# Performance work log

Hardware: AMD Instinct MI355X
Metric: run time of the kernel (lower is better)

The kernel has to match this reference:

```python
import jax, jax.numpy as jnp
import numpy as np

N_FFT = 200; HOP = 100; N_FREQ = N_FFT // 2 + 1  # 101
EMB = 256; HEADS = 8; DHEAD = EMB // HEADS; DEPTH = 4
N_CH = 23; B = 256; TS = 2000
MASK_RATIO = 0.9


def _layernorm(x, s, b):
    mu = jnp.mean(x, -1, keepdims=True)
    var = jnp.mean((x - mu) ** 2, -1, keepdims=True)
    return (x - mu) * jax.lax.rsqrt(var + 1e-5) * s + b


def _posenc(T, d):
    pos = jnp.arange(T, dtype=jnp.float32)[:, None]
    div = jnp.exp(jnp.arange(0, d, 2, dtype=jnp.float32) * (-np.log(10000.0) / d))
    pe = jnp.zeros((T, d), jnp.float32)
    pe = pe.at[:, 0::2].set(jnp.sin(pos * div))
    pe = pe.at[:, 1::2].set(jnp.cos(pos * div))
    return pe


def setup_inputs() -> dict:
    key = jax.random.key(0)
    ks = jax.random.split(key, 12)
    def n(k, shape):
        return (jax.random.normal(k, shape) * 0.02).astype(jnp.float32)
    T = 1 + (TS - N_FFT) // HOP  # 19
    S = N_CH * T                 # 437
    return dict(
        x=jax.random.normal(ks[0], (B, N_CH, TS), jnp.float32),
        mask_noise=jax.random.uniform(ks[1], (B, S, EMB), dtype=jnp.float32),
        W_proj=n(ks[2], (N_FREQ, EMB)), b_proj=jnp.zeros((EMB,), jnp.float32),
        channel_tokens=n(ks[3], (N_CH, EMB)),
        ln1_s=jnp.ones((DEPTH, EMB), jnp.float32), ln1_b=jnp.zeros((DEPTH, EMB), jnp.float32),
        Wq=n(ks[4], (DEPTH, EMB, EMB)), Wk=n(ks[5], (DEPTH, EMB, EMB)),
        Wv=n(ks[6], (DEPTH, EMB, EMB)), Wo=n(ks[7], (DEPTH, EMB, EMB)),
        bo=jnp.zeros((DEPTH, EMB), jnp.float32),
        ln2_s=jnp.ones((DEPTH, EMB), jnp.float32), ln2_b=jnp.zeros((DEPTH, EMB), jnp.float32),
        W1=n(ks[8], (DEPTH, EMB, 4 * EMB)), b1=jnp.zeros((DEPTH, 4 * EMB), jnp.float32),
        W2=n(ks[9], (DEPTH, 4 * EMB, EMB)), b2=jnp.zeros((DEPTH, EMB), jnp.float32),
    )


def _forward(x, mask_noise, W_proj, b_proj, channel_tokens,
             ln1_s, ln1_b, Wq, Wk, Wv, Wo, bo, ln2_s, ln2_b, W1, b1, W2, b2):
    Bb, C, ts = x.shape
    T = 1 + (ts - N_FFT) // HOP
    # ---- vectorized per-channel STFT (rect window, center=False, onesided) ----
    idx = jnp.arange(T)[:, None] * HOP + jnp.arange(N_FFT)[None, :]  # [T, n_fft]
    frames = x[:, :, idx]                                            # [B,C,T,n_fft]
    spec = jnp.abs(jnp.fft.rfft(frames, axis=-1)).astype(x.dtype)    # [B,C,T,F]
    # patch embedding (Linear over freq), channel token, positional encoding
    emb = spec @ W_proj + b_proj                                     # [B,C,T,E]
    emb = emb + channel_tokens[:C][None, :, None, :]
    emb = emb + _posenc(T, emb.shape[-1])[None, None]
    emb = emb.reshape(Bb, C * T, -1)                                 # [B,S,E]
    # ---- random masking (mask_ratio=0.9 as hard-coded in forward) ----
    mask = mask_noise < MASK_RATIO
    masked = jnp.where(mask, jnp.zeros((), emb.dtype), emb)
    # ---- LinearAttentionTransformer (non-causal linear attention, pre-norm) ----
    h = masked
    for l in range(DEPTH):
        y = _layernorm(h, ln1_s[l], ln1_b[l])
        S = y.shape[1]
        q = (y @ Wq[l]).reshape(Bb, S, HEADS, DHEAD).transpose(0, 2, 1, 3)
        k = (y @ Wk[l]).reshape(Bb, S, HEADS, DHEAD).transpose(0, 2, 1, 3)
        v = (y @ Wv[l]).reshape(Bb, S, HEADS, DHEAD).transpose(0, 2, 1, 3)
        q = jax.nn.softmax(q, axis=-1) * (DHEAD ** -0.5)
        k = jax.nn.softmax(k, axis=2)  # softmax over sequence
        ctx = jnp.einsum('bhnd,bhne->bhde', k, v)     # [B,H,d,d] global context
        att = jnp.einsum('bhnd,bhde->bhne', q, ctx)   # [B,H,S,d]
        att = att.transpose(0, 2, 1, 3).reshape(Bb, S, EMB)
        h = h + att @ Wo[l] + bo[l]
        y = _layernorm(h, ln2_s[l], ln2_b[l])
        h = h + jax.nn.gelu(y @ W1[l] + b1[l]) @ W2[l] + b2[l]
    return emb, masked, h, mask


def reference(x, mask_noise, W_proj, b_proj, channel_tokens,
              ln1_s, ln1_b, Wq, Wk, Wv, Wo, bo, ln2_s, ln2_b, W1, b1, W2, b2):
    return _forward(x, mask_noise, W_proj, b_proj, channel_tokens,
                    ln1_s, ln1_b, Wq, Wk, Wv, Wo, bo, ln2_s, ln2_b, W1, b1, W2, b2)
```

## Files before the change

kernel.cpp:

```cpp
#include <hip/hip_runtime.h>

#define BB    256
#define NCH   23
#define TT    19
#define SS    437
#define BSR   111872
#define EMBD  256
#define NHEAD 8
#define DH    32
#define NFREQ 101
#define NFFT  200
#define HOPSZ 100
#define TSLEN 2000
#define HID   1024
#define NDEPTH 4
#define NTOK  28639232
#define QKVW  768
#define WL    786432

typedef __attribute__((ext_vector_type(8))) __bf16 bf16x8;
typedef __attribute__((ext_vector_type(4))) float  f32x4;

__device__ __forceinline__ float gelu_f(float x){
    return 0.5f*x*(1.0f + tanhf(0.7978845608028654f*(x + 0.044715f*x*x*x)));
}
__device__ __forceinline__ unsigned short f2b(float f){
    unsigned u = __float_as_uint(f);
    return (unsigned short)((u + 0x7FFFu + ((u >> 16) & 1u)) >> 16);
}
__device__ __forceinline__ float b2f(unsigned short h){
    return __uint_as_float(((unsigned)h) << 16);
}

__device__ __forceinline__ void swz_tile(int& bx, int& by){
    int nx = gridDim.x, nwg = nx * gridDim.y;
    int lid = blockIdx.y * nx + blockIdx.x;
    int q = nwg >> 3, r = nwg & 7;
    int xcd = lid & 7, off = lid >> 3;
    int wgid = (xcd < r ? xcd*(q+1) : r*(q+1) + (xcd-r)*q) + off;
    bx = wgid % nx; by = wgid / nx;
}

__global__ void init_twb(unsigned short* __restrict__ tw){
    int i = blockIdx.x*256 + threadIdx.x;
    if(i >= 256*256) return;
    int n = i >> 8, k = i & 255;
    float v = 0.f;
    if(k < NFFT){
        if(n <= 100){
            int ph = (n * k) % NFFT;
            v = cosf(6.283185307179586f * (float)ph / (float)NFFT);
        } else if(n >= 128 && n <= 228){
            int ph = ((n - 128) * k) % NFFT;
            v = sinf(6.283185307179586f * (float)ph / (float)NFFT);
        }
    }
    tw[i] = f2b(v);
}

__global__ void init_pe(float* __restrict__ pe){
    int i = blockIdx.x*256 + threadIdx.x;
    if(i >= TT*EMBD) return;
    int t = i / EMBD, e = i % EMBD;
    int j = e >> 1;
    float div = expf((float)(2*j) * (-9.210340371976184f/256.0f));
    float ang = (float)t * div;
    pe[i] = (e & 1) ? cosf(ang) : sinf(ang);
}

__global__ void wprep_proj(const float* __restrict__ Wp, unsigned short* __restrict__ Wt){
    int i = blockIdx.x*256 + threadIdx.x;
    if(i >= 256*128) return;
    int e = i >> 7, k = i & 127;
    Wt[i] = f2b(k < NFREQ ? Wp[(size_t)k*EMBD + e] : 0.f);
}

__global__ void wprep_qkv(const float* __restrict__ Wq, const float* __restrict__ Wk,
                          const float* __restrict__ Wv, unsigned short* __restrict__ wbuf){
    long i = (long)blockIdx.x*256 + threadIdx.x;
    if(i >= (long)NDEPTH*QKVW*EMBD) return;
    int l = (int)(i / (QKVW*EMBD));
    int rem = (int)(i % (QKVW*EMBD));
    int n = rem >> 8, k = rem & 255;
    const float* W = (n < 256) ? Wq : (n < 512) ? Wk : Wv;
    wbuf[(size_t)l*WL + rem] = f2b(W[(size_t)l*65536 + (size_t)k*256 + (n & 255)]);
}
__global__ void wprep_wo(const float* __restrict__ Wo, unsigned short* __restrict__ wbuf){
    int i = blockIdx.x*256 + threadIdx.x;
    if(i >= NDEPTH*65536) return;
    int l = i >> 16, rem = i & 65535;
    int n = rem >> 8, k = rem & 255;
    wbuf[(size_t)l*WL + 196608 + rem] = f2b(Wo[(size_t)l*65536 + (size_t)k*256 + n]);
}
__global__ void wprep_w1(const float* __restrict__ W1, unsigned short* __restrict__ wbuf){
    long i = (long)blockIdx.x*256 + threadIdx.x;
    if(i >= (long)NDEPTH*262144) return;
    int l = (int)(i >> 18), rem = (int)(i & 262143);
    int n = rem >> 8, k = rem & 255;
    wbuf[(size_t)l*WL + 262144 + rem] = f2b(W1[(size_t)l*262144 + (size_t)k*1024 + n]);
}
__global__ void wprep_w2(const float* __restrict__ W2, unsigned short* __restrict__ wbuf){
    long i = (long)blockIdx.x*256 + threadIdx.x;
    if(i >= (long)NDEPTH*262144) return;
    int l = (int)(i >> 18), rem = (int)(i & 262143);
    int n = rem >> 10, k = rem & 1023;
    wbuf[(size_t)l*WL + 524288 + rem] = f2b(W2[(size_t)l*262144 + (size_t)k*256 + n]);
}

__global__ void frames_bf16(const float* __restrict__ x, unsigned short* __restrict__ fr){
    for(long i = (long)blockIdx.x*blockDim.x + threadIdx.x; i < (long)BSR*256;
        i += (long)gridDim.x*blockDim.x){
        int  k   = (int)(i & 255);
        long row = i >> 8;
        int  t   = (int)(row % TT);
        long bc  = row / TT;
        float v = (k < NFFT) ? x[bc*(long)TSLEN + (long)t*HOPSZ + k] : 0.f;
        fr[i] = f2b(v);
    }
}

__global__ void combine_bf16(const float* __restrict__ dft, unsigned short* __restrict__ sp){
    for(long i = (long)blockIdx.x*blockDim.x + threadIdx.x; i < (long)BSR*128;
        i += (long)gridDim.x*blockDim.x){
        int  f   = (int)(i & 127);
        long row = i >> 7;
        float v = 0.f;
        if(f < NFREQ){
            float c = dft[row*256 + f];
            float s = dft[row*256 + 128 + f];
            v = sqrtf(c*c + s*s);
        }
        sp[i] = f2b(v);
    }
}

template<int MODE>
__global__ __launch_bounds__(256) void gemm_mfma(
    const unsigned short* __restrict__ A, const unsigned short* __restrict__ Bt,
    const float* __restrict__ bias, void* __restrict__ Cv,
    const float* __restrict__ Cin, int M, int N, int K)
{
    __shared__ __align__(16) unsigned short As[128*64];
    __shared__ __align__(16) unsigned short Bs[128*64];
    const int tid = threadIdx.x;
    const int w = tid >> 6, l = tid & 63;
    int bx, by; swz_tile(bx, by);
    const int m0 = by * 128, n0 = bx * 128;
    const int wr = w >> 1, wc = w & 1;
    f32x4 acc[4][4];
    #pragma unroll
    for(int i=0;i<4;++i)
        #pragma unroll
        for(int jj=0;jj<4;++jj) acc[i][jj] = (f32x4){0.f,0.f,0.f,0.f};

    const int srow0 = w*32 + (l>>3);
    const int sgrp  = l & 7;

    for(int k0 = 0; k0 < K; k0 += 64){
        #pragma unroll
        for(int it=0; it<4; ++it){
            int row  = srow0 + it*8;
            int colA = ((sgrp ^ (row & 7)) << 3);
            const unsigned short* ga = A  + (size_t)(m0+row)*K + k0 + colA;
            const unsigned short* gb = Bt + (size_t)(n0+row)*K + k0 + colA;
            __builtin_amdgcn_global_load_lds(
                (__attribute__((address_space(1))) void*)ga,
                (__attribute__((address_space(3))) void*)(As + w*2048 + it*512),
                16, 0, 0);
            __builtin_amdgcn_global_load_lds(
                (__attribute__((address_space(1))) void*)gb,
                (__attribute__((address_space(3))) void*)(Bs + w*2048 + it*512),
                16, 0, 0);
        }
        __syncthreads();
        #pragma unroll
        for(int kk=0; kk<2; ++kk){
            bf16x8 af[4], bfr[4];
            #pragma unroll
            for(int mi=0;mi<4;++mi){
                int row = wr*64 + mi*16 + (l & 15);
                int grp = kk*4 + (l >> 4);
                af[mi] = *(const bf16x8*)&As[row*64 + ((grp ^ (row&7))<<3)];
            }
            #pragma unroll
            for(int ni=0;ni<4;++ni){
                int row = wc*64 + ni*16 + (l & 15);
                int grp = kk*4 + (l >> 4);
                bfr[ni] = *(const bf16x8*)&Bs[row*64 + ((grp ^ (row&7))<<3)];
            }
            #pragma unroll
            for(int mi=0;mi<4;++mi)
                #pragma unroll
                for(int ni=0;ni<4;++ni)
                    acc[mi][ni] = __builtin_amdgcn_mfma_f32_16x16x32_bf16(
                        af[mi], bfr[ni], acc[mi][ni], 0, 0, 0);
        }
        __syncthreads();
    }
    const int cn  = l & 15;
    const int cr4 = (l >> 4) * 4;
    if(MODE == 2 || MODE == 3){
        unsigned short* C = (unsigned short*)Cv;
        #pragma unroll
        for(int ni=0;ni<4;++ni){
            int n = n0 + wc*64 + ni*16 + cn;
            float bn = (MODE==2) ? bias[n] : 0.f;
            #pragma unroll
            for(int mi=0;mi<4;++mi){
                int mB = m0 + wr*64 + mi*16 + cr4;
                #pragma unroll
                for(int r=0;r<4;++r){
                    float v = acc[mi][ni][r];
                    C[(size_t)(mB+r)*N + n] = f2b(MODE==2 ? gelu_f(v + bn) : v);
                }
            }
        }
    } else {
        float* C = (float*)Cv;
        #pragma unroll
        for(int ni=0;ni<4;++ni){
            int n = n0 + wc*64 + ni*16 + cn;
            float bn = (MODE==1) ? bias[n] : 0.0f;
            #pragma unroll
            for(int mi=0;mi<4;++mi){
                int mB = m0 + wr*64 + mi*16 + cr4;
                #pragma unroll
                for(int r=0;r<4;++r){
                    size_t off = (size_t)(mB+r)*N + n;
                    if(MODE==0) C[off] = acc[mi][ni][r];
                    else        C[off] = Cin[off] + acc[mi][ni][r] + bn;
                }
            }
        }
    }
}

__global__ __launch_bounds__(256) void gemm_emb(
    const unsigned short* __restrict__ A, const unsigned short* __restrict__ Bt,
    const float* __restrict__ bp, const float* __restrict__ ctok,
    const float* __restrict__ pe, const float* __restrict__ noise,
    float* __restrict__ o_emb, float* __restrict__ o_masked,
    float* __restrict__ o_mask, float* __restrict__ bufH)
{
    const int K = 128, N = 256;
    __shared__ __align__(16) unsigned short As[128*64];
    __shared__ __align__(16) unsigned short Bs[128*64];
    const int tid = threadIdx.x;
    const int w = tid >> 6, l = tid & 63;
    int bx, by; swz_tile(bx, by);
    const int m0 = by * 128, n0 = bx * 128;
    const int wr = w >> 1, wc = w & 1;
    f32x4 acc[4][4];
    #pragma unroll
    for(int i=0;i<4;++i)
        #pragma unroll
        for(int jj=0;jj<4;++jj) acc[i][jj] = (f32x4){0.f,0.f,0.f,0.f};
    const int srow0 = w*32 + (l>>3);
    const int sgrp  = l & 7;
    for(int k0 = 0; k0 < K; k0 += 64){
        #pragma unroll
        for(int it=0; it<4; ++it){
            int row  = srow0 + it*8;
            int colA = ((sgrp ^ (row & 7)) << 3);
            const unsigned short* ga = A  + (size_t)(m0+row)*K + k0 + colA;
            const unsigned short* gb = Bt + (size_t)(n0+row)*K + k0 + colA;
            __builtin_amdgcn_global_load_lds(
                (__attribute__((address_space(1))) void*)ga,
                (__attribute__((address_space(3))) void*)(As + w*2048 + it*512),
                16, 0, 0);
            __builtin_amdgcn_global_load_lds(
                (__attribute__((address_space(1))) void*)gb,
                (__attribute__((address_space(3))) void*)(Bs + w*2048 + it*512),
                16, 0, 0);
        }
        __syncthreads();
        #pragma unroll
        for(int kk=0; kk<2; ++kk){
            bf16x8 af[4], bfr[4];
            #pragma unroll
            for(int mi=0;mi<4;++mi){
                int row = wr*64 + mi*16 + (l & 15);
                int grp = kk*4 + (l >> 4);
                af[mi] = *(const bf16x8*)&As[row*64 + ((grp ^ (row&7))<<3)];
            }
            #pragma unroll
            for(int ni=0;ni<4;++ni){
                int row = wc*64 + ni*16 + (l & 15);
                int grp = kk*4 + (l >> 4);
                bfr[ni] = *(const bf16x8*)&Bs[row*64 + ((grp ^ (row&7))<<3)];
            }
            #pragma unroll
            for(int mi=0;mi<4;++mi)
                #pragma unroll
                for(int ni=0;ni<4;++ni)
                    acc[mi][ni] = __builtin_amdgcn_mfma_f32_16x16x32_bf16(
                        af[mi], bfr[ni], acc[mi][ni], 0, 0, 0);
        }
        __syncthreads();
    }
    const int cn  = l & 15;
    const int cr4 = (l >> 4) * 4;
    #pragma unroll
    for(int ni=0;ni<4;++ni){
        int n = n0 + wc*64 + ni*16 + cn;
        float bn = bp[n];
        #pragma unroll
        for(int mi=0;mi<4;++mi){
            int mB = m0 + wr*64 + mi*16 + cr4;
            #pragma unroll
            for(int r=0;r<4;++r){
                int m = mB + r;
                int t = m % TT;
                int c = (m / TT) % NCH;
                size_t off = (size_t)m*EMBD + n;
                float v = acc[mi][ni][r] + bn + ctok[c*EMBD + n] + pe[t*EMBD + n];
                o_emb[off] = v;
                float mn = noise[off];
                bool  msk = mn < 0.9f;
                float md = msk ? 0.f : v;
                bufH[off]     = md;
                o_masked[off] = md;
                o_mask[off]   = msk ? 1.f : 0.f;
            }
        }
    }
}

__global__ __launch_bounds__(256) void ln_bf16(const float* __restrict__ X,
    const float* __restrict__ s, const float* __restrict__ b,
    unsigned short* __restrict__ Y)
{
    int w = threadIdx.x >> 6, lane = threadIdx.x & 63;
    long row = (long)blockIdx.x*4 + w;
    const float* xr = X + row*EMBD;
    float4 v = *(const float4*)(xr + lane*4);
    float sum = v.x + v.y + v.z + v.w;
    #pragma unroll
    for(int o=32;o>0;o>>=1) sum += __shfl_xor(sum, o, 64);
    float mu = sum * (1.0f/256.0f);
    float dx = v.x-mu, dy = v.y-mu, dz = v.z-mu, dw = v.w-mu;
    float vs = dx*dx + dy*dy + dz*dz + dw*dw;
    #pragma unroll
    for(int o=32;o>0;o>>=1) vs += __shfl_xor(vs, o, 64);
    float rstd = rsqrtf(vs*(1.0f/256.0f) + 1e-5f);
    float4 s4 = *(const float4*)(s + lane*4);
    float4 b4 = *(const float4*)(b + lane*4);
    ushort4 o4;
    o4.x = f2b(dx*rstd*s4.x + b4.x);
    o4.y = f2b(dy*rstd*s4.y + b4.y);
    o4.z = f2b(dz*rstd*s4.z + b4.z);
    o4.w = f2b(dw*rstd*s4.w + b4.w);
    *(ushort4*)(Y + row*EMBD + lane*4) = o4;
}

__global__ __launch_bounds__(256) void colstats(const unsigned short* __restrict__ qkvb,
                         float* __restrict__ kmax, float* __restrict__ ksum)
{
    __shared__ float sm[8][32], ss[8][32];
    int b = blockIdx.x;
    int c = blockIdx.y*32 + (threadIdx.x & 31);
    int g = threadIdx.x >> 5;
    const unsigned short* p = qkvb + (size_t)b*SS*QKVW + 256 + c;
    float m = -1e30f, s = 0.f;
    for(int n = g; n < SS; n += 8){
        float xv = b2f(p[(size_t)n*QKVW]);
        if(xv > m){ s = s*expf(m-xv) + 1.f; m = xv; }
        else      { s += expf(xv-m); }
    }
    sm[g][threadIdx.x & 31] = m;
    ss[g][threadIdx.x & 31] = s;
    __syncthreads();
    if(g == 0){
        int lc = threadIdx.x & 31;
        float M = m, S = s;
        #pragma unroll
        for(int o = 1; o < 8; ++o){
            float m2 = sm[o][lc], s2 = ss[o][lc];
            if(m2 > M){ S = S*expf(M-m2) + s2; M = m2; }
            else      { S += s2*expf(m2-M); }
        }
        kmax[b*EMBD + c] = M;
        ksum[b*EMBD + c] = S;
    }
}

__global__ __launch_bounds__(256) void ctx_kernel(const unsigned short* __restrict__ qkvb,
    const float* __restrict__ kmax, const float* __restrict__ ksum,
    float* __restrict__ ctx)
{
    __shared__ float kt[16][DH], vt[16][DH];
    int bh = blockIdx.x; int b = bh >> 3, h = bh & 7;
    int tid = threadIdx.x;
    int d = tid >> 3, e4 = (tid & 7) * 4;
    float km = kmax[b*EMBD + h*DH + d];
    float a0=0,a1=0,a2=0,a3=0;
    for(int n0=0;n0<SS;n0+=16){
        __syncthreads();
        #pragma unroll
        for(int i=0;i<2;++i){
            int e = tid + i*256;
            int nn = e >> 5, dd = e & 31;
            int n = n0 + nn;
            float kv, vv;
            if(n < SS){
                size_t off = ((size_t)(b*SS+n))*QKVW + h*DH + dd;
                kv = b2f(qkvb[off + 256]);
                vv = b2f(qkvb[off + 512]);
            } else { kv = -1e30f; vv = 0.f; }
            kt[nn][dd] = kv; vt[nn][dd] = vv;
        }
        __syncthreads();
        #pragma unroll
        for(int nn=0;nn<16;++nn){
            float ke = expf(kt[nn][d] - km);
            a0 = fmaf(ke, vt[nn][e4+0], a0);
            a1 = fmaf(ke, vt[nn][e4+1], a1);
            a2 = fmaf(ke, vt[nn][e4+2], a2);
            a3 = fmaf(ke, vt[nn][e4+3], a3);
        }
    }
    float inv = 1.0f / ksum[b*EMBD + h*DH + d];
    float* op = ctx + ((size_t)bh*DH + d)*DH + e4;
    op[0]=a0*inv; op[1]=a1*inv; op[2]=a2*inv; op[3]=a3*inv;
}

__global__ __launch_bounds__(256) void att_kernel(const unsigned short* __restrict__ qkvb,
    const float* __restrict__ ctx, unsigned short* __restrict__ att)
{
    __shared__ float qs[4][EMBD];
    int w = threadIdx.x >> 6, lane = threadIdx.x & 63;
    int b = blockIdx.y;
    int s = blockIdx.x*4 + w;
    if(s >= SS) return;
    long row = (long)b*SS + s;
    ushort4 qu = *(const ushort4*)(qkvb + (size_t)row*QKVW + lane*4);
    float4 q4 = make_float4(b2f(qu.x), b2f(qu.y), b2f(qu.z), b2f(qu.w));
    float m = fmaxf(fmaxf(q4.x,q4.y), fmaxf(q4.z,q4.w));
    #pragma unroll
    for(int o=1;o<8;o<<=1) m = fmaxf(m, __shfl_xor(m, o, 64));
    float e0 = expf(q4.x-m), e1 = expf(q4.y-m), e2 = expf(q4.z-m), e3 = expf(q4.w-m);
    float ssum = e0+e1+e2+e3;
    #pragma unroll
    for(int o=1;o<8;o<<=1) ssum += __shfl_xor(ssum, o, 64);
    float sc = 0.17677669529663687f / ssum;
    *(float4*)&qs[w][lane*4] = make_float4(e0*sc, e1*sc, e2*sc, e3*sc);
    int head = lane >> 3;
    int ecol = (lane & 7) * 4;
    const float* cb = ctx + ((size_t)(b*NHEAD + head))*DH*DH + ecol;
    float a0=0,a1=0,a2=0,a3=0;
    #pragma unroll
    for(int d=0; d<DH; ++d){
        float qd = qs[w][head*DH + d];
        float4 c4 = *(const float4*)(cb + d*DH);
        a0 = fmaf(qd, c4.x, a0);
        a1 = fmaf(qd, c4.y, a1);
        a2 = fmaf(qd, c4.z, a2);
        a3 = fmaf(qd, c4.w, a3);
    }
    ushort4 o4; o4.x=f2b(a0); o4.y=f2b(a1); o4.z=f2b(a2); o4.w=f2b(a3);
    *(ushort4*)(att + row*EMBD + lane*4) = o4;
}

extern "C" void kernel_launch(void* const* d_in, const int* in_sizes, int n_in,
                              void* d_out, int out_size, void* d_ws, size_t ws_size,
                              hipStream_t stream)
{
    if(n_in != 18) return;

    const float* x     = (const float*)d_in[0];
    const float* noise = (const float*)d_in[1];
    const float* Wproj = (const float*)d_in[2];
    const float* bproj = (const float*)d_in[3];
    const float* ctok  = (const float*)d_in[4];
    const float* ln1s  = (const float*)d_in[5];
    const float* ln1b  = (const float*)d_in[6];
    const float* Wq    = (const float*)d_in[7];
    const float* Wk    = (const float*)d_in[8];
    const float* Wv    = (const float*)d_in[9];
    const float* Wo    = (const float*)d_in[10];
    const float* bo    = (const float*)d_in[11];
    const float* ln2s  = (const float*)d_in[12];
    const float* ln2b  = (const float*)d_in[13];
    const float* W1    = (const float*)d_in[14];
    const float* b1    = (const float*)d_in[15];
    const float* W2    = (const float*)d_in[16];
    const float* b2    = (const float*)d_in[17];

    float* ws   = (float*)d_ws;
    float* bufH = ws;
    float* big  = ws + (size_t)NTOK;
    unsigned short* qkvb   = (unsigned short*)big;
    float*          dftout = big;
    unsigned short* hidb   = (unsigned short*)big;
    unsigned short* specb  = (unsigned short*)(big + (size_t)NTOK);
    unsigned short* bufYb  = (unsigned short*)(big + 2*(size_t)NTOK);
    unsigned short* framesb= bufYb;
    unsigned short* attb   = bufYb;
    float* kmax = (float*)(bufYb + (size_t)NTOK);
    float* ksum = kmax + BB*EMBD;
    float* ctxb = ksum + BB*EMBD;
    float* peb  = ctxb + (size_t)BB*NHEAD*DH*DH;
    unsigned short* twb  = (unsigned short*)(peb + TT*EMBD);
    unsigned short* Wpb  = twb + 65536;
    unsigned short* wbuf = Wpb + 32768;
    size_t need_bytes = ((char*)(wbuf + 4*(size_t)WL)) - (char*)d_ws;
    if(ws_size < need_bytes) return;

    float* out      = (float*)d_out;
    float* o_emb    = out;
    float* o_masked = out + (size_t)NTOK;
    float* o_h      = out + 2*(size_t)NTOK;
    float* o_mask   = out + 3*(size_t)NTOK;

    dim3 blk(256);

    init_twb<<<256, blk, 0, stream>>>(twb);
    init_pe <<<19,  blk, 0, stream>>>(peb);
    wprep_proj<<<128, blk, 0, stream>>>(Wproj, Wpb);
    wprep_qkv<<<3072, blk, 0, stream>>>(Wq, Wk, Wv, wbuf);
    wprep_wo <<<1024, blk, 0, stream>>>(Wo, wbuf);
    wprep_w1 <<<4096, blk, 0, stream>>>(W1, wbuf);
    wprep_w2 <<<4096, blk, 0, stream>>>(W2, wbuf);

    frames_bf16<<<4096, blk, 0, stream>>>(x, framesb);
    gemm_mfma<0><<<dim3(2,874), blk, 0, stream>>>(framesb, twb, nullptr, dftout,
                                                  nullptr, BSR, 256, 256);
    combine_bf16<<<4096, blk, 0, stream>>>(dftout, specb);
    gemm_emb<<<dim3(2,874), blk, 0, stream>>>(specb, Wpb, bproj, ctok, peb, noise,
                                              o_emb, o_masked, o_mask, bufH);

    for(int l=0;l<NDEPTH;++l){
        unsigned short* wl   = wbuf + (size_t)l*WL;
        unsigned short* Wqkv = wl;
        unsigned short* Wot  = wl + 196608;
        unsigned short* W1t  = wl + 262144;
        unsigned short* W2t  = wl + 524288;

        ln_bf16<<<BSR/4, blk, 0, stream>>>(bufH, ln1s + l*EMBD, ln1b + l*EMBD, bufYb);
        gemm_mfma<3><<<dim3(6,874), blk, 0, stream>>>(bufYb, Wqkv, nullptr, qkvb,
                                                      nullptr, BSR, QKVW, EMBD);
        colstats<<<dim3(BB,8), blk, 0, stream>>>(qkvb, kmax, ksum);
        ctx_kernel<<<BB*NHEAD, blk, 0, stream>>>(qkvb, kmax, ksum, ctxb);
        att_kernel<<<dim3(110, BB), blk, 0, stream>>>(qkvb, ctxb, attb);
        gemm_mfma<1><<<dim3(2,874), blk, 0, stream>>>(attb, Wot, bo + l*EMBD, bufH,
                                                      bufH, BSR, EMBD, EMBD);
        ln_bf16<<<BSR/4, blk, 0, stream>>>(bufH, ln2s + l*EMBD, ln2b + l*EMBD, bufYb);
        gemm_mfma<2><<<dim3(8,874), blk, 0, stream>>>(bufYb, W1t, b1 + l*HID, hidb,
                                                      nullptr, BSR, HID, EMBD);
        float* cOut = (l == NDEPTH-1) ? o_h : bufH;
        gemm_mfma<1><<<dim3(2,874), blk, 0, stream>>>(hidb, W2t, b2 + l*EMBD, cOut,
                                                      bufH, BSR, EMBD, HID);
    }
}
```

Baseline: 3.535 ms.

## Store residual stream in bf16, fuse DFT magnitude and column stats

The residual stream buffer changes from fp32 to bf16, so layernorm reads and the residual-add GEMM epilogues move half the bytes. The DFT twiddle rows are interleaved as cos/sin so the GEMM epilogue can form magnitudes with a lane shuffle, which removes the fp32 DFT output and the separate combine kernel. The key softmax column statistics are computed inside the context kernel, which removes the colstats launch and its round trip through global memory. Rounding the residual to bf16 between layers costs accuracy and may fail tolerance checks.

```diff
diff --git a/kernel.cpp b/kernel.cpp
--- a/kernel.cpp
+++ b/kernel.cpp
@@ -46,14 +46,11 @@
     if(i >= 256*256) return;
     int n = i >> 8, k = i & 255;
     float v = 0.f;
-    if(k < NFFT){
-        if(n <= 100){
-            int ph = (n * k) % NFFT;
-            v = cosf(6.283185307179586f * (float)ph / (float)NFFT);
-        } else if(n >= 128 && n <= 228){
-            int ph = ((n - 128) * k) % NFFT;
-            v = sinf(6.283185307179586f * (float)ph / (float)NFFT);
-        }
+    if(k < NFFT && n < 2*NFREQ){
+        int f = n >> 1;
+        int ph = (f * k) % NFFT;
+        float ang = 6.283185307179586f * (float)ph / (float)NFFT;
+        v = (n & 1) ? sinf(ang) : cosf(ang);
     }
     tw[i] = f2b(v);
 }
@@ -119,26 +116,61 @@
     }
 }
 
-__global__ void combine_bf16(const float* __restrict__ dft, unsigned short* __restrict__ sp){
-    for(long i = (long)blockIdx.x*blockDim.x + threadIdx.x; i < (long)BSR*128;
-        i += (long)gridDim.x*blockDim.x){
-        int  f   = (int)(i & 127);
-        long row = i >> 7;
-        float v = 0.f;
-        if(f < NFREQ){
-            float c = dft[row*256 + f];
-            float s = dft[row*256 + 128 + f];
-            v = sqrtf(c*c + s*s);
-        }
-        sp[i] = f2b(v);
-    }
-}
+#define GEMM_CORE(A_, B_, K_) \
+    f32x4 acc[4][4]; \
+    _Pragma("unroll") \
+    for(int i=0;i<4;++i) \
+        _Pragma("unroll") \
+        for(int jj=0;jj<4;++jj) acc[i][jj] = (f32x4){0.f,0.f,0.f,0.f}; \
+    const int srow0 = w*32 + (l>>3); \
+    const int sgrp  = l & 7; \
+    for(int k0 = 0; k0 < (K_); k0 += 64){ \
+        _Pragma("unroll") \
+        for(int it=0; it<4; ++it){ \
+            int row  = srow0 + it*8; \
+            int colA = ((sgrp ^ (row & 7)) << 3); \
+            const unsigned short* ga = (A_) + (size_t)(m0+row)*(K_) + k0 + colA; \
+            const unsigned short* gb = (B_) + (size_t)(n0+row)*(K_) + k0 + colA; \
+            __builtin_amdgcn_global_load_lds( \
+                (__attribute__((address_space(1))) void*)ga, \
+                (__attribute__((address_space(3))) void*)(As + w*2048 + it*512), \
+                16, 0, 0); \
+            __builtin_amdgcn_global_load_lds( \
+                (__attribute__((address_space(1))) void*)gb, \
+                (__attribute__((address_space(3))) void*)(Bs + w*2048 + it*512), \
+                16, 0, 0); \
+        } \
+        __syncthreads(); \
+        _Pragma("unroll") \
+        for(int kk=0; kk<2; ++kk){ \
+            bf16x8 af[4], bfr[4]; \
+            _Pragma("unroll") \
+            for(int mi=0;mi<4;++mi){ \
+                int row = wr*64 + mi*16 + (l & 15); \
+                int grp = kk*4 + (l >> 4); \
+                af[mi] = *(const bf16x8*)&As[row*64 + ((grp ^ (row&7))<<3)]; \
+            } \
+            _Pragma("unroll") \
+            for(int ni=0;ni<4;++ni){ \
+                int row = wc*64 + ni*16 + (l & 15); \
+                int grp = kk*4 + (l >> 4); \
+                bfr[ni] = *(const bf16x8*)&Bs[row*64 + ((grp ^ (row&7))<<3)]; \
+            } \
+            _Pragma("unroll") \
+            for(int mi=0;mi<4;++mi) \
+                _Pragma("unroll") \
+                for(int ni=0;ni<4;++ni) \
+                    acc[mi][ni] = __builtin_amdgcn_mfma_f32_16x16x32_bf16( \
+                        af[mi], bfr[ni], acc[mi][ni], 0, 0, 0); \
+        } \
+        __syncthreads(); \
+    }
 
 template<int MODE>
 __global__ __launch_bounds__(256) void gemm_mfma(
     const unsigned short* __restrict__ A, const unsigned short* __restrict__ Bt,
     const float* __restrict__ bias, void* __restrict__ Cv,
-    const float* __restrict__ Cin, int M, int N, int K)
+    const unsigned short* __restrict__ Cin, int M, int N, int K)
 {
     __shared__ __align__(16) unsigned short As[128*64];
     __shared__ __align__(16) unsigned short Bs[128*64];
@@ -147,88 +179,62 @@
     int bx, by; swz_tile(bx, by);
     const int m0 = by * 128, n0 = bx * 128;
     const int wr = w >> 1, wc = w & 1;
-    f32x4 acc[4][4];
-    #pragma unroll
-    for(int i=0;i<4;++i)
-        #pragma unroll
-        for(int jj=0;jj<4;++jj) acc[i][jj] = (f32x4){0.f,0.f,0.f,0.f};
-
-    const int srow0 = w*32 + (l>>3);
-    const int sgrp  = l & 7;
-
-    for(int k0 = 0; k0 < K; k0 += 64){
-        #pragma unroll
-        for(int it=0; it<4; ++it){
-            int row  = srow0 + it*8;
-            int colA = ((sgrp ^ (row & 7)) << 3);
-            const unsigned short* ga = A  + (size_t)(m0+row)*K + k0 + colA;
-            const unsigned short* gb = Bt + (size_t)(n0+row)*K + k0 + colA;
-            __builtin_amdgcn_global_load_lds(
-                (__attribute__((address_space(1))) void*)ga,
-                (__attribute__((address_space(3))) void*)(As + w*2048 + it*512),
-                16, 0, 0);
-            __builtin_amdgcn_global_load_lds(
-                (__attribute__((address_space(1))) void*)gb,
-                (__attribute__((address_space(3))) void*)(Bs + w*2048 + it*512),
-                16, 0, 0);
-        }
-        __syncthreads();
-        #pragma unroll
-        for(int kk=0; kk<2; ++kk){
-            bf16x8 af[4], bfr[4];
-            #pragma unroll
-            for(int mi=0;mi<4;++mi){
-                int row = wr*64 + mi*16 + (l & 15);
-                int grp = kk*4 + (l >> 4);
-                af[mi] = *(const bf16x8*)&As[row*64 + ((grp ^ (row&7))<<3)];
-            }
-            #pragma unroll
-            for(int ni=0;ni<4;++ni){
-                int row = wc*64 + ni*16 + (l & 15);
-                int grp = kk*4 + (l >> 4);
-                bfr[ni] = *(const bf16x8*)&Bs[row*64 + ((grp ^ (row&7))<<3)];
-            }
-            #pragma unroll
-            for(int mi=0;mi<4;++mi)
-                #pragma unroll
-                for(int ni=0;ni<4;++ni)
-                    acc[mi][ni] = __builtin_amdgcn_mfma_f32_16x16x32_bf16(
-                        af[mi], bfr[ni], acc[mi][ni], 0, 0, 0);
-        }
-        __syncthreads();
-    }
+    GEMM_CORE(A, Bt, K)
     const int cn  = l & 15;
     const int cr4 = (l >> 4) * 4;
-    if(MODE == 2 || MODE == 3){
-        unsigned short* C = (unsigned short*)Cv;
+    #pragma unroll
+    for(int ni=0;ni<4;++ni){
+        int n = n0 + wc*64 + ni*16 + cn;
+        float bn = (MODE==1 || MODE==2 || MODE==4) ? bias[n] : 0.f;
         #pragma unroll
-        for(int ni=0;ni<4;++ni){
-            int n = n0 + wc*64 + ni*16 + cn;
-            float bn = (MODE==2) ? bias[n] : 0.f;
+        for(int mi=0;mi<4;++mi){
+            int mB = m0 + wr*64 + mi*16 + cr4;
             #pragma unroll
-            for(int mi=0;mi<4;++mi){
-                int mB = m0 + wr*64 + mi*16 + cr4;
-                #pragma unroll
-                for(int r=0;r<4;++r){
-                    float v = acc[mi][ni][r];
-                    C[(size_t)(mB+r)*N + n] = f2b(MODE==2 ? gelu_f(v + bn) : v);
+            for(int r=0;r<4;++r){
+                size_t off = (size_t)(mB+r)*N + n;
+                float v = acc[mi][ni][r];
+                if(MODE == 1){
+                    ((unsigned short*)Cv)[off] = f2b(b2f(Cin[off]) + v + bn);
+                } else if(MODE == 2){
+                    ((unsigned short*)Cv)[off] = f2b(gelu_f(v + bn));
+                } else if(MODE == 3){
+                    ((unsigned short*)Cv)[off] = f2b(v);
+                } else {
+                    ((float*)Cv)[off] = b2f(Cin[off]) + v + bn;
                 }
             }
         }
-    } else {
-        float* C = (float*)Cv;
+    }
+}
+
+__global__ __launch_bounds__(256) void gemm_dft(
+    const unsigned short* __restrict__ A, const unsigned short* __restrict__ Bt,
+    unsigned short* __restrict__ spec)
+{
+    const int K = 256;
+    __shared__ __align__(16) unsigned short As[128*64];
+    __shared__ __align__(16) unsigned short Bs[128*64];
+    const int tid = threadIdx.x;
+    const int w = tid >> 6, l = tid & 63;
+    int bx, by; swz_tile(bx, by);
+    const int m0 = by * 128, n0 = bx * 128;
+    const int wr = w >> 1, wc = w & 1;
+    GEMM_CORE(A, Bt, K)
+    const int cn  = l & 15;
+    const int cr4 = (l >> 4) * 4;
+    #pragma unroll
+    for(int ni=0;ni<4;++ni){
+        int n = n0 + wc*64 + ni*16 + cn;
         #pragma unroll
-        for(int ni=0;ni<4;++ni){
-            int n = n0 + wc*64 + ni*16 + cn;
-            float bn = (MODE==1) ? bias[n] : 0.0f;
+        for(int mi=0;mi<4;++mi){
+            int mB = m0 + wr*64 + mi*16 + cr4;
             #pragma unroll
-            for(int mi=0;mi<4;++mi){
-                int mB = m0 + wr*64 + mi*16 + cr4;
-                #pragma unroll
-                for(int r=0;r<4;++r){
-                    size_t off = (size_t)(mB+r)*N + n;
-                    if(MODE==0) C[off] = acc[mi][ni][r];
-                    else        C[off] = Cin[off] + acc[mi][ni][r] + bn;
+            for(int r=0;r<4;++r){
+                float own = acc[mi][ni][r];
+                float par = __shfl_xor(own, 1, 64);
+                if(!(cn & 1)){
+                    float sv = sqrtf(own*own + par*par);
+                    spec[(size_t)(mB+r)*128 + (n >> 1)] = f2b(sv);
                 }
             }
         }
@@ -240,7 +246,7 @@
     const float* __restrict__ bp, const float* __restrict__ ctok,
     const float* __restrict__ pe, const float* __restrict__ noise,
     float* __restrict__ o_emb, float* __restrict__ o_masked,
-    float* __restrict__ o_mask, float* __restrict__ bufH)
+    float* __restrict__ o_mask, unsigned short* __restrict__ bufH)
 {
     const int K = 128, N = 256;
     __shared__ __align__(16) unsigned short As[128*64];
@@ -250,54 +256,7 @@
     int bx, by; swz_tile(bx, by);
     const int m0 = by * 128, n0 = bx * 128;
     const int wr = w >> 1, wc = w & 1;
-    f32x4 acc[4][4];
-    #pragma unroll
-    for(int i=0;i<4;++i)
-        #pragma unroll
-        for(int jj=0;jj<4;++jj) acc[i][jj] = (f32x4){0.f,0.f,0.f,0.f};
-    const int srow0 = w*32 + (l>>3);
-    const int sgrp  = l & 7;
-    for(int k0 = 0; k0 < K; k0 += 64){
-        #pragma unroll
-        for(int it=0; it<4; ++it){
-            int row  = srow0 + it*8;
-            int colA = ((sgrp ^ (row & 7)) << 3);
-            const unsigned short* ga = A  + (size_t)(m0+row)*K + k0 + colA;
-            const unsigned short* gb = Bt + (size_t)(n0+row)*K + k0 + colA;
-            __builtin_amdgcn_global_load_lds(
-                (__attribute__((address_space(1))) void*)ga,
-                (__attribute__((address_space(3))) void*)(As + w*2048 + it*512),
-                16, 0, 0);
-            __builtin_amdgcn_global_load_lds(
-                (__attribute__((address_space(1))) void*)gb,
-                (__attribute__((address_space(3))) void*)(Bs + w*2048 + it*512),
-                16, 0, 0);
-        }
-        __syncthreads();
-        #pragma unroll
-        for(int kk=0; kk<2; ++kk){
-            bf16x8 af[4], bfr[4];
-            #pragma unroll
-            for(int mi=0;mi<4;++mi){
-                int row = wr*64 + mi*16 + (l & 15);
-                int grp = kk*4 + (l >> 4);
-                af[mi] = *(const bf16x8*)&As[row*64 + ((grp ^ (row&7))<<3)];
-            }
-            #pragma unroll
-            for(int ni=0;ni<4;++ni){
-                int row = wc*64 + ni*16 + (l & 15);
-                int grp = kk*4 + (l >> 4);
-                bfr[ni] = *(const bf16x8*)&Bs[row*64 + ((grp ^ (row&7))<<3)];
-            }
-            #pragma unroll
-            for(int mi=0;mi<4;++mi)
-                #pragma unroll
-                for(int ni=0;ni<4;++ni)
-                    acc[mi][ni] = __builtin_amdgcn_mfma_f32_16x16x32_bf16(
-                        af[mi], bfr[ni], acc[mi][ni], 0, 0, 0);
-        }
-        __syncthreads();
-    }
+    GEMM_CORE(A, Bt, K)
     const int cn  = l & 15;
     const int cr4 = (l >> 4) * 4;
     #pragma unroll
@@ -318,7 +277,7 @@
                 float mn = noise[off];
                 bool  msk = mn < 0.9f;
                 float md = msk ? 0.f : v;
-                bufH[off]     = md;
+                bufH[off]     = f2b(md);
                 o_masked[off] = md;
                 o_mask[off]   = msk ? 1.f : 0.f;
             }
@@ -326,19 +285,19 @@
     }
 }
 
-__global__ __launch_bounds__(256) void ln_bf16(const float* __restrict__ X,
+__global__ __launch_bounds__(256) void ln_bf16(const unsigned short* __restrict__ X,
     const float* __restrict__ s, const float* __restrict__ b,
     unsigned short* __restrict__ Y)
 {
     int w = threadIdx.x >> 6, lane = threadIdx.x & 63;
     long row = (long)blockIdx.x*4 + w;
-    const float* xr = X + row*EMBD;
-    float4 v = *(const float4*)(xr + lane*4);
-    float sum = v.x + v.y + v.z + v.w;
+    ushort4 u = *(const ushort4*)(X + row*EMBD + lane*4);
+    float x0 = b2f(u.x), x1 = b2f(u.y), x2 = b2f(u.z), x3 = b2f(u.w);
+    float sum = x0 + x1 + x2 + x3;
     #pragma unroll
     for(int o=32;o>0;o>>=1) sum += __shfl_xor(sum, o, 64);
     float mu = sum * (1.0f/256.0f);
-    float dx = v.x-mu, dy = v.y-mu, dz = v.z-mu, dw = v.w-mu;
+    float dx = x0-mu, dy = x1-mu, dz = x2-mu, dw = x3-mu;
     float vs = dx*dx + dy*dy + dz*dz + dw*dw;
     #pragma unroll
     for(int o=32;o>0;o>>=1) vs += __shfl_xor(vs, o, 64);
@@ -353,46 +312,41 @@
     *(ushort4*)(Y + row*EMBD + lane*4) = o4;
 }
 
-__global__ __launch_bounds__(256) void colstats(const unsigned short* __restrict__ qkvb,
-                         float* __restrict__ kmax, float* __restrict__ ksum)
-{
+__global__ __launch_bounds__(256) void ctx_kernel(const unsigned short* __restrict__ qkvb,
+    float* __restrict__ ctx)
+{
+    __shared__ float kt[16][DH], vt[16][DH];
     __shared__ float sm[8][32], ss[8][32];
-    int b = blockIdx.x;
-    int c = blockIdx.y*32 + (threadIdx.x & 31);
-    int g = threadIdx.x >> 5;
-    const unsigned short* p = qkvb + (size_t)b*SS*QKVW + 256 + c;
-    float m = -1e30f, s = 0.f;
-    for(int n = g; n < SS; n += 8){
-        float xv = b2f(p[(size_t)n*QKVW]);
-        if(xv > m){ s = s*expf(m-xv) + 1.f; m = xv; }
-        else      { s += expf(xv-m); }
-    }
-    sm[g][threadIdx.x & 31] = m;
-    ss[g][threadIdx.x & 31] = s;
+    __shared__ float kmsL[32], kinvL[32];
+    int bh = blockIdx.x; int b = bh >> 3, h = bh & 7;
+    int tid = threadIdx.x;
+
+    {
+        int d = tid & 31, g = tid >> 5;
+        const unsigned short* p = qkvb + (size_t)b*SS*QKVW + 256 + h*DH + d;
+        float m = -1e30f, s = 0.f;
+        for(int n = g; n < SS; n += 8){
+            float xv = b2f(p[(size_t)n*QKVW]);
+            if(xv > m){ s = s*expf(m-xv) + 1.f; m = xv; }
+            else      { s += expf(xv-m); }
+        }
+        sm[g][d] = m; ss[g][d] = s;
+    }
     __syncthreads();
-    if(g == 0){
-        int lc = threadIdx.x & 31;
-        float M = m, S = s;
+    if(tid < 32){
+        float M = sm[0][tid], S = ss[0][tid];
         #pragma unroll
         for(int o = 1; o < 8; ++o){
-            float m2 = sm[o][lc], s2 = ss[o][lc];
+            float m2 = sm[o][tid], s2 = ss[o][tid];
             if(m2 > M){ S = S*expf(M-m2) + s2; M = m2; }
             else      { S += s2*expf(m2-M); }
         }
-        kmax[b*EMBD + c] = M;
-        ksum[b*EMBD + c] = S;
-    }
-}
-
-__global__ __launch_bounds__(256) void ctx_kernel(const unsigned short* __restrict__ qkvb,
-    const float* __restrict__ kmax, const float* __restrict__ ksum,
-    float* __restrict__ ctx)
-{
-    __shared__ float kt[16][DH], vt[16][DH];
-    int bh = blockIdx.x; int b = bh >> 3, h = bh & 7;
-    int tid = threadIdx.x;
+        kmsL[tid] = M; kinvL[tid] = 1.0f / S;
+    }
+    __syncthreads();
+
     int d = tid >> 3, e4 = (tid & 7) * 4;
-    float km = kmax[b*EMBD + h*DH + d];
+    float km = kmsL[d];
     float a0=0,a1=0,a2=0,a3=0;
     for(int n0=0;n0<SS;n0+=16){
         __syncthreads();
@@ -419,7 +373,7 @@
             a3 = fmaf(ke, vt[nn][e4+3], a3);
         }
     }
-    float inv = 1.0f / ksum[b*EMBD + h*DH + d];
+    float inv = kinvL[d];
     float* op = ctx + ((size_t)bh*DH + d)*DH + e4;
     op[0]=a0*inv; op[1]=a1*inv; op[2]=a2*inv; op[3]=a3*inv;
 }
@@ -486,25 +440,21 @@
     const float* W2    = (const float*)d_in[16];
     const float* b2    = (const float*)d_in[17];
 
-    float* ws   = (float*)d_ws;
-    float* bufH = ws;
-    float* big  = ws + (size_t)NTOK;
+    char* p = (char*)d_ws;
+    unsigned short* bufHb = (unsigned short*)p;           p += (size_t)NTOK*2;
+    float* big = (float*)p;                               p += (size_t)NTOK*2*4;
     unsigned short* qkvb   = (unsigned short*)big;
-    float*          dftout = big;
     unsigned short* hidb   = (unsigned short*)big;
-    unsigned short* specb  = (unsigned short*)(big + (size_t)NTOK);
-    unsigned short* bufYb  = (unsigned short*)(big + 2*(size_t)NTOK);
+    unsigned short* specb  = (unsigned short*)p;          p += (size_t)BSR*128*2;
+    unsigned short* bufYb  = (unsigned short*)p;          p += (size_t)NTOK*2;
     unsigned short* framesb= bufYb;
     unsigned short* attb   = bufYb;
-    float* kmax = (float*)(bufYb + (size_t)NTOK);
-    float* ksum = kmax + BB*EMBD;
-    float* ctxb = ksum + BB*EMBD;
-    float* peb  = ctxb + (size_t)BB*NHEAD*DH*DH;
-    unsigned short* twb  = (unsigned short*)(peb + TT*EMBD);
-    unsigned short* Wpb  = twb + 65536;
-    unsigned short* wbuf = Wpb + 32768;
-    size_t need_bytes = ((char*)(wbuf + 4*(size_t)WL)) - (char*)d_ws;
-    if(ws_size < need_bytes) return;
+    float* ctxb = (float*)p;                              p += (size_t)BB*NHEAD*DH*DH*4;
+    float* peb  = (float*)p;                              p += (size_t)TT*EMBD*4;
+    unsigned short* twb  = (unsigned short*)p;            p += (size_t)65536*2;
+    unsigned short* Wpb  = (unsigned short*)p;            p += (size_t)32768*2;
+    unsigned short* wbuf = (unsigned short*)p;            p += (size_t)4*WL*2;
+    if(ws_size < (size_t)(p - (char*)d_ws)) return;
 
     float* out      = (float*)d_out;
     float* o_emb    = out;
@@ -523,11 +473,9 @@
     wprep_w2 <<<4096, blk, 0, stream>>>(W2, wbuf);
 
     frames_bf16<<<4096, blk, 0, stream>>>(x, framesb);
-    gemm_mfma<0><<<dim3(2,874), blk, 0, stream>>>(framesb, twb, nullptr, dftout,
-                                                  nullptr, BSR, 256, 256);
-    combine_bf16<<<4096, blk, 0, stream>>>(dftout, specb);
+    gemm_dft<<<dim3(2,874), blk, 0, stream>>>(framesb, twb, specb);
     gemm_emb<<<dim3(2,874), blk, 0, stream>>>(specb, Wpb, bproj, ctok, peb, noise,
-                                              o_emb, o_masked, o_mask, bufH);
+                                              o_emb, o_masked, o_mask, bufHb);
 
     for(int l=0;l<NDEPTH;++l){
         unsigned short* wl   = wbuf + (size_t)l*WL;
@@ -536,19 +484,21 @@
         unsigned short* W1t  = wl + 262144;
         unsigned short* W2t  = wl + 524288;
 
-        ln_bf16<<<BSR/4, blk, 0, stream>>>(bufH, ln1s + l*EMBD, ln1b + l*EMBD, bufYb);
+        ln_bf16<<<BSR/4, blk, 0, stream>>>(bufHb, ln1s + l*EMBD, ln1b + l*EMBD, bufYb);
         gemm_mfma<3><<<dim3(6,874), blk, 0, stream>>>(bufYb, Wqkv, nullptr, qkvb,
                                                       nullptr, BSR, QKVW, EMBD);
-        colstats<<<dim3(BB,8), blk, 0, stream>>>(qkvb, kmax, ksum);
-        ctx_kernel<<<BB*NHEAD, blk, 0, stream>>>(qkvb, kmax, ksum, ctxb);
+        ctx_kernel<<<BB*NHEAD, blk, 0, stream>>>(qkvb, ctxb);
         att_kernel<<<dim3(110, BB), blk, 0, stream>>>(qkvb, ctxb, attb);
-        gemm_mfma<1><<<dim3(2,874), blk, 0, stream>>>(attb, Wot, bo + l*EMBD, bufH,
-                                                      bufH, BSR, EMBD, EMBD);
-        ln_bf16<<<BSR/4, blk, 0, stream>>>(bufH, ln2s + l*EMBD, ln2b + l*EMBD, bufYb);
+        gemm_mfma<1><<<dim3(2,874), blk, 0, stream>>>(attb, Wot, bo + l*EMBD, bufHb,
+                                                      bufHb, BSR, EMBD, EMBD);
+        ln_bf16<<<BSR/4, blk, 0, stream>>>(bufHb, ln2s + l*EMBD, ln2b + l*EMBD, bufYb);
         gemm_mfma<2><<<dim3(8,874), blk, 0, stream>>>(bufYb, W1t, b1 + l*HID, hidb,
                                                       nullptr, BSR, HID, EMBD);
-        float* cOut = (l == NDEPTH-1) ? o_h : bufH;
-        gemm_mfma<1><<<dim3(2,874), blk, 0, stream>>>(hidb, W2t, b2 + l*EMBD, cOut,
-                                                      bufH, BSR, EMBD, HID);
-    }
-}
+        if(l == NDEPTH-1)
+            gemm_mfma<4><<<dim3(2,874), blk, 0, stream>>>(hidb, W2t, b2 + l*EMBD, o_h,
+                                                          bufHb, BSR, EMBD, HID);
+        else
+            gemm_mfma<1><<<dim3(2,874), blk, 0, stream>>>(hidb, W2t, b2 + l*EMBD, bufHb,
+                                                          bufHb, BSR, EMBD, HID);
+    }
+}
```

Result: faster. 3.305 ms (-6.5%).
